# Kernel optimization log

Hardware: AMD Instinct MI355X
Metric: run time of the kernel (lower is better)

## Reference

```python
import jax, jax.numpy as jnp
import numpy as np

N_STATE = 1280
N_HEAD = 20
D_HEAD = N_STATE // N_HEAD  # 64
N_MLP = 4 * N_STATE         # 5120
EPS = 1e-5


def _layer_norm(x, gamma, beta):
    mu = jnp.mean(x, axis=-1, keepdims=True)
    var = jnp.mean(jnp.square(x - mu), axis=-1, keepdims=True)
    return (x - mu) * jax.lax.rsqrt(var + EPS) * gamma + beta


def setup_inputs() -> dict:
    key = jax.random.key(0)
    ks = jax.random.split(key, 16)
    s = lambda fan_in: 1.0 / np.sqrt(fan_in)
    d = {
        "x": jax.random.normal(ks[0], (1, 1500, N_STATE), jnp.float32),
        # attention projections (stored [in, out]; torch Linear does x @ W.T + b)
        "Wq": jax.random.normal(ks[1], (N_STATE, N_STATE), jnp.float32) * s(N_STATE),
        "bq": jax.random.normal(ks[2], (N_STATE,), jnp.float32) * 0.02,
        "Wk": jax.random.normal(ks[3], (N_STATE, N_STATE), jnp.float32) * s(N_STATE),  # no bias
        "Wv": jax.random.normal(ks[4], (N_STATE, N_STATE), jnp.float32) * s(N_STATE),
        "bv": jax.random.normal(ks[5], (N_STATE,), jnp.float32) * 0.02,
        "Wo": jax.random.normal(ks[6], (N_STATE, N_STATE), jnp.float32) * s(N_STATE),
        "bo": jax.random.normal(ks[7], (N_STATE,), jnp.float32) * 0.02,
        # layer norms
        "ln1_g": jnp.ones((N_STATE,), jnp.float32),
        "ln1_b": jnp.zeros((N_STATE,), jnp.float32),
        "ln2_g": jnp.ones((N_STATE,), jnp.float32),
        "ln2_b": jnp.zeros((N_STATE,), jnp.float32),
        # MLP
        "W1": jax.random.normal(ks[8], (N_STATE, N_MLP), jnp.float32) * s(N_STATE),
        "b1": jax.random.normal(ks[9], (N_MLP,), jnp.float32) * 0.02,
        "W2": jax.random.normal(ks[10], (N_MLP, N_STATE), jnp.float32) * s(N_MLP),
        "b2": jax.random.normal(ks[11], (N_STATE,), jnp.float32) * 0.02,
    }
    return d


def reference(x, Wq, bq, Wk, Wv, bv, Wo, bo, ln1_g, ln1_b, ln2_g, ln2_b, W1, b1, W2, b2):
    B, S, C = x.shape
    scale = D_HEAD ** -0.5

    # --- multi-head self-attention ---
    h = _layer_norm(x, ln1_g, ln1_b)
    q = (h @ Wq + bq).reshape(B, S, N_HEAD, D_HEAD)
    k = (h @ Wk).reshape(B, S, N_HEAD, D_HEAD)
    v = (h @ Wv + bv).reshape(B, S, N_HEAD, D_HEAD)
    # scores: [B, H, Q, K]; softmax over keys (dim=1 'k' in the torch einsum)
    scores = jnp.einsum('bqhd,bkhd->bhqk', q, k) * scale
    w = jax.nn.softmax(scores, axis=-1)
    attn = jnp.einsum('bhqk,bkhd->bqhd', w, v).reshape(B, S, C)
    attn = attn @ Wo + bo
    x = x + attn

    # --- MLP (exact GELU, matching torch nn.GELU default) ---
    h2 = _layer_norm(x, ln2_g, ln2_b)
    h2 = jax.nn.gelu(h2 @ W1 + b1, approximate=False)
    x = x + (h2 @ W2 + b2)
    return x
```

## Files before the change

### kernel.cpp

```cpp
#include <hip/hip_runtime.h>
#include <hip/hip_bf16.h>
#include <math.h>

typedef __bf16 bf16x8 __attribute__((ext_vector_type(8)));
typedef float f32x4 __attribute__((ext_vector_type(4)));

#define SEQ 1500
#define CDIM 1280
#define NHEAD 20
#define DHEAD 64
#define NMLP 5120
#define QKVN 3840
#define VTLD 1504
#define APAD 68

#define GLOAD_LDS16(gp, lp)                                                    \
  __builtin_amdgcn_global_load_lds(                                            \
      (const __attribute__((address_space(1))) unsigned int*)(gp),             \
      (__attribute__((address_space(3))) unsigned int*)(lp), 16, 0, 0)

__global__ __launch_bounds__(256) void pack_params_kernel(
    const unsigned int* __restrict__ xw, const void* bq, const void* bv,
    const void* bo, const void* g1, const void* be1, const void* g2,
    const void* be2, const void* b1, const void* b2,
    __bf16* __restrict__ pb, int* __restrict__ flag) {
  __shared__ int cnt[256];
  const unsigned int w = xw[threadIdx.x];
  const unsigned int e = (w >> 7) & 0xFF;
  cnt[threadIdx.x] = (e >= 100 && e <= 150) ? 1 : 0;
  __syncthreads();
  for (int s = 128; s > 0; s >>= 1) {
    if (threadIdx.x < (unsigned)s) cnt[threadIdx.x] += cnt[threadIdx.x + s];
    __syncthreads();
  }
  const int isbf = (cnt[0] >= 160) ? 1 : 0;
  if (blockIdx.x == 0 && threadIdx.x == 0) flag[0] = isbf;
  const int i = blockIdx.x * 256 + threadIdx.x;
  if (i >= 16640) return;
  auto ld = [&](const void* p, int j) -> float {
    return isbf ? (float)((const __bf16*)p)[j] : ((const float*)p)[j];
  };
  float v;
  if (i < 3840) {
    if (i < 1280) v = ld(bq, i);
    else if (i < 2560) v = 0.f;
    else v = ld(bv, i - 2560);
  } else if (i < 5120) v = ld(bo, i - 3840);
  else if (i < 6400) v = ld(g1, i - 5120);
  else if (i < 7680) v = ld(be1, i - 6400);
  else if (i < 8960) v = ld(g2, i - 7680);
  else if (i < 10240) v = ld(be2, i - 8960);
  else if (i < 15360) v = ld(b1, i - 10240);
  else v = ld(b2, i - 15360);
  pb[i] = (__bf16)v;
}

__device__ __forceinline__ void transpose_body(const void* in, __bf16* out,
                                               int K, int N, int isbf,
                                               int bx, int by) {
  __shared__ __bf16 t[32][33];
  const int tx = threadIdx.x, ty = threadIdx.y;
  const int n0 = bx * 32, k0 = by * 32;
  if (isbf) {
    const __bf16* s = (const __bf16*)in;
#pragma unroll
    for (int i = ty; i < 32; i += 8)
      t[i][tx] = s[(size_t)(k0 + i) * N + n0 + tx];
  } else {
    const float* s = (const float*)in;
#pragma unroll
    for (int i = ty; i < 32; i += 8)
      t[i][tx] = (__bf16)s[(size_t)(k0 + i) * N + n0 + tx];
  }
  __syncthreads();
#pragma unroll
  for (int i = ty; i < 32; i += 8)
    out[(size_t)(n0 + i) * K + k0 + tx] = t[tx][i];
}

__global__ __launch_bounds__(256) void transpose_all_kernel(
    const void* Wq, const void* Wk, const void* Wv, const void* Wo,
    const void* W1, const void* W2, __bf16* __restrict__ Wqkvt,
    __bf16* __restrict__ Wot, __bf16* __restrict__ W1t,
    __bf16* __restrict__ W2t, const int* __restrict__ flag) {
  const int id = blockIdx.x;
  const int isbf = flag[0];
  if (id < 6400) {
    const int w = id / 1600, r = id % 1600;
    const void* in = (w == 0) ? Wq : (w == 1) ? Wk : (w == 2) ? Wv : Wo;
    __bf16* out = (w < 3) ? (Wqkvt + (size_t)w * CDIM * CDIM) : Wot;
    transpose_body(in, out, CDIM, CDIM, isbf, r % 40, r / 40);
  } else if (id < 12800) {
    const int r = id - 6400;
    transpose_body(W1, W1t, CDIM, NMLP, isbf, r % 160, r / 160);
  } else {
    const int r = id - 12800;
    transpose_body(W2, W2t, NMLP, CDIM, isbf, r % 40, r / 40);
  }
}

__global__ __launch_bounds__(256) void transpose_act_kernel(const __bf16* __restrict__ in,
                                                            __bf16* __restrict__ out,
                                                            int istride) {
  __shared__ __bf16 t[32][33];
  const int tx = threadIdx.x, ty = threadIdx.y;
  const int n0 = blockIdx.x * 32, k0 = blockIdx.y * 32;
#pragma unroll
  for (int i = ty; i < 32; i += 8) {
    const int k = k0 + i;
    t[i][tx] = (k < SEQ) ? in[(size_t)k * istride + n0 + tx] : (__bf16)0.f;
  }
  __syncthreads();
#pragma unroll
  for (int i = ty; i < 32; i += 8) {
    const int kk = k0 + tx;
    if (kk < VTLD) out[(size_t)(n0 + i) * VTLD + kk] = t[tx][i];
  }
}

__global__ __launch_bounds__(256) void ln_kernel(const void* __restrict__ X,
                                                 const __bf16* __restrict__ gamma,
                                                 const __bf16* __restrict__ beta,
                                                 __bf16* __restrict__ Y,
                                                 const int* __restrict__ flag) {
  const int isf32 = (flag[0] == 0);
  const int row = blockIdx.x;
  float v[5];
  float s = 0.f, s2 = 0.f;
#pragma unroll
  for (int i = 0; i < 5; ++i) {
    const int c = threadIdx.x + 256 * i;
    const size_t idx = (size_t)row * CDIM + c;
    v[i] = isf32 ? ((const float*)X)[idx] : (float)((const __bf16*)X)[idx];
    s += v[i];
    s2 += v[i] * v[i];
  }
  const int lane = threadIdx.x & 63, wv = threadIdx.x >> 6;
#pragma unroll
  for (int off = 32; off > 0; off >>= 1) {
    s += __shfl_down(s, off);
    s2 += __shfl_down(s2, off);
  }
  __shared__ float red[8];
  if (lane == 0) { red[wv] = s; red[4 + wv] = s2; }
  __syncthreads();
  s = red[0] + red[1] + red[2] + red[3];
  s2 = red[4] + red[5] + red[6] + red[7];
  const float mu = s * (1.f / CDIM);
  const float var = s2 * (1.f / CDIM) - mu * mu;
  const float rstd = rsqrtf(fmaxf(var, 0.f) + 1e-5f);
#pragma unroll
  for (int i = 0; i < 5; ++i) {
    const int c = threadIdx.x + 256 * i;
    Y[(size_t)row * CDIM + c] =
        (__bf16)((v[i] - mu) * rstd * (float)gamma[c] + (float)beta[c]);
  }
}

__global__ __launch_bounds__(256) void resid_ln_kernel(
    const float* __restrict__ P, const __bf16* __restrict__ bo,
    const void* __restrict__ X, const __bf16* __restrict__ gamma,
    const __bf16* __restrict__ beta, __bf16* __restrict__ X1,
    __bf16* __restrict__ H2, const int* __restrict__ flag) {
  const int isf32 = (flag[0] == 0);
  const int row = blockIdx.x;
  const int MN = SEQ * CDIM;
  float v[5];
  float s = 0.f, s2 = 0.f;
#pragma unroll
  for (int i = 0; i < 5; ++i) {
    const int c = threadIdx.x + 256 * i;
    const size_t idx = (size_t)row * CDIM + c;
    const float xv = isf32 ? ((const float*)X)[idx] : (float)((const __bf16*)X)[idx];
    const float val = P[idx] + P[MN + idx] + (float)bo[c] + xv;
    X1[idx] = (__bf16)val;
    v[i] = val;
    s += val;
    s2 += val * val;
  }
  const int lane = threadIdx.x & 63, wv = threadIdx.x >> 6;
#pragma unroll
  for (int off = 32; off > 0; off >>= 1) {
    s += __shfl_down(s, off);
    s2 += __shfl_down(s2, off);
  }
  __shared__ float red[8];
  if (lane == 0) { red[wv] = s; red[4 + wv] = s2; }
  __syncthreads();
  s = red[0] + red[1] + red[2] + red[3];
  s2 = red[4] + red[5] + red[6] + red[7];
  const float mu = s * (1.f / CDIM);
  const float var = s2 * (1.f / CDIM) - mu * mu;
  const float rstd = rsqrtf(fmaxf(var, 0.f) + 1e-5f);
#pragma unroll
  for (int i = 0; i < 5; ++i) {
    const int c = threadIdx.x + 256 * i;
    H2[(size_t)row * CDIM + c] =
        (__bf16)((v[i] - mu) * rstd * (float)gamma[c] + (float)beta[c]);
  }
}

__global__ __launch_bounds__(256) void gemm64_kernel(
    const __bf16* __restrict__ A, const __bf16* __restrict__ Bt,
    const __bf16* __restrict__ bias, void* __restrict__ Cv,
    int M, int N, int K, int KS, int gelu, int nsplit) {
  __shared__ __bf16 As[2][64 * 32];
  __shared__ __bf16 Bs[2][128 * 32];
  const int bm = blockIdx.x, bn = blockIdx.y, sz = blockIdx.z;
  const int tid = threadIdx.x;
  const int lane = tid & 63, wave = tid >> 6;
  const int l16 = lane & 15, kq = (lane >> 4) << 3;
  const int lrow = lane >> 2, lcol = (lane & 3) << 3;
  const int wn = wave * 32;

  f32x4 acc[4][2];
  const f32x4 zero = {0.f, 0.f, 0.f, 0.f};
#pragma unroll
  for (int i = 0; i < 4; ++i)
#pragma unroll
    for (int j = 0; j < 2; ++j) acc[i][j] = zero;

  const int kbeg = sz * KS;
  int kend = kbeg + KS;
  if (kend > K) kend = K;

  int ga = bm * 64 + wave * 16 + lrow;
  if (ga > M - 1) ga = M - 1;
  const __bf16* Ap = A + (size_t)ga * K + lcol;

  for (int k0 = kbeg; k0 < kend; k0 += 64) {
#pragma unroll
    for (int c = 0; c < 2; ++c)
      GLOAD_LDS16(Ap + k0 + c * 32, &As[c][wave * 512]);
#pragma unroll
    for (int c = 0; c < 2; ++c)
#pragma unroll
      for (int t = 0; t < 2; ++t) {
        const int seg = t * 4 + wave;
        const int gb = bn * 128 + seg * 16 + lrow;
        GLOAD_LDS16(Bt + (size_t)gb * K + k0 + c * 32 + lcol, &Bs[c][seg * 512]);
      }
    __syncthreads();
    bf16x8 af[4][2], bfr[2][2];
#pragma unroll
    for (int i = 0; i < 4; ++i)
#pragma unroll
      for (int c = 0; c < 2; ++c)
        af[i][c] = *(const bf16x8*)(&As[c][(i * 16 + l16) * 32 + kq]);
#pragma unroll
    for (int j = 0; j < 2; ++j)
#pragma unroll
      for (int c = 0; c < 2; ++c)
        bfr[j][c] = *(const bf16x8*)(&Bs[c][(wn + j * 16 + l16) * 32 + kq]);
#pragma unroll
    for (int i = 0; i < 4; ++i)
#pragma unroll
      for (int j = 0; j < 2; ++j)
#pragma unroll
        for (int c = 0; c < 2; ++c)
          acc[i][j] = __builtin_amdgcn_mfma_f32_16x16x32_bf16(af[i][c], bfr[j][c],
                                                              acc[i][j], 0, 0, 0);
    __syncthreads();
  }

  const int rq4 = (lane >> 4) * 4;
  if (nsplit > 1) {
    float* P = (float*)Cv + (size_t)sz * M * N;
#pragma unroll
    for (int i = 0; i < 4; ++i)
#pragma unroll
      for (int r = 0; r < 4; ++r) {
        const int grow = bm * 64 + i * 16 + rq4 + r;
        if (grow >= M) continue;
#pragma unroll
        for (int j = 0; j < 2; ++j) {
          const int gcol = bn * 128 + wn + j * 16 + l16;
          P[(size_t)grow * N + gcol] = acc[i][j][r];
        }
      }
  } else {
    __bf16* Cb = (__bf16*)Cv;
#pragma unroll
    for (int i = 0; i < 4; ++i)
#pragma unroll
      for (int r = 0; r < 4; ++r) {
        const int grow = bm * 64 + i * 16 + rq4 + r;
        if (grow >= M) continue;
#pragma unroll
        for (int j = 0; j < 2; ++j) {
          const int gcol = bn * 128 + wn + j * 16 + l16;
          float vv = acc[i][j][r];
          if (bias) vv += (float)bias[gcol];
          if (gelu) vv = 0.5f * vv * (1.f + erff(vv * 0.70710678118654752f));
          Cb[(size_t)grow * N + gcol] = (__bf16)vv;
        }
      }
  }
}

__global__ __launch_bounds__(256, 2) void gemm128c_kernel(
    const __bf16* __restrict__ A, const __bf16* __restrict__ Bt,
    const __bf16* __restrict__ bias, __bf16* __restrict__ C,
    int M, int N, int K, int gelu, int mtiles) {
  __shared__ __bf16 As[2][128 * 64];
  __shared__ __bf16 Bs[2][128 * 64];

  const int nwg = mtiles * (N >> 7);
  const int qq = nwg >> 3, rr = nwg & 7;
  const int xcd = blockIdx.x & 7, rk = blockIdx.x >> 3;
  const int wg = (xcd < rr ? xcd * (qq + 1) : rr * (qq + 1) + (xcd - rr) * qq) + rk;
  const int bm = wg % mtiles, bn = wg / mtiles;

  const int tid = threadIdx.x;
  const int lane = tid & 63, wave = tid >> 6;
  const int wm = (wave >> 1) * 64, wn = (wave & 1) * 64;
  const int l16 = lane & 15, quad = lane >> 4;

  const int rT = tid >> 3, sl = tid & 7;
  const int aoff = ((sl * 16) ^ ((rT & 7) << 4)) >> 1;
  const __bf16* Ap[4];
  const __bf16* Bp[4];
#pragma unroll
  for (int s = 0; s < 4; ++s) {
    int gm = bm * 128 + s * 32 + rT;
    if (gm > M - 1) gm = M - 1;
    Ap[s] = A + (size_t)gm * K + aoff;
    Bp[s] = Bt + (size_t)(bn * 128 + s * 32 + rT) * K + aoff;
  }
  const int ldst = tid * 8;

  const int xsw = (l16 & 7) << 4;
  const int kb0 = ((quad << 4) ^ xsw) >> 1;
  const int kb1 = (((quad << 4) + 64) ^ xsw) >> 1;

  f32x4 acc[4][4];
  const f32x4 zero = {0.f, 0.f, 0.f, 0.f};
#pragma unroll
  for (int i = 0; i < 4; ++i)
#pragma unroll
    for (int j = 0; j < 4; ++j) acc[i][j] = zero;

  const int NT = K >> 6;

#define STAGE128(b, k0)                                       \
  do {                                                        \
    _Pragma("unroll")                                         \
    for (int s = 0; s < 4; ++s) {                             \
      GLOAD_LDS16(Ap[s] + (k0), &As[b][s * 2048 + ldst]);     \
      GLOAD_LDS16(Bp[s] + (k0), &Bs[b][s * 2048 + ldst]);     \
    }                                                         \
  } while (0)

  STAGE128(0, 0);
  for (int t = 0; t < NT; ++t) {
    const int cur = t & 1;
    if (t + 1 < NT) {
      STAGE128(cur ^ 1, (t + 1) * 64);
      asm volatile("s_waitcnt vmcnt(8)" ::: "memory");
    } else {
      asm volatile("s_waitcnt vmcnt(0)" ::: "memory");
    }
    __builtin_amdgcn_s_barrier();
    __builtin_amdgcn_sched_barrier(0);
    bf16x8 af[4][2], bfr[4][2];
#pragma unroll
    for (int i = 0; i < 4; ++i) {
      const int row = (wm + i * 16 + l16) * 64;
      af[i][0] = *(const bf16x8*)(&As[cur][row + kb0]);
      af[i][1] = *(const bf16x8*)(&As[cur][row + kb1]);
    }
#pragma unroll
    for (int j = 0; j < 4; ++j) {
      const int row = (wn + j * 16 + l16) * 64;
      bfr[j][0] = *(const bf16x8*)(&Bs[cur][row + kb0]);
      bfr[j][1] = *(const bf16x8*)(&Bs[cur][row + kb1]);
    }
    __builtin_amdgcn_s_setprio(1);
#pragma unroll
    for (int i = 0; i < 4; ++i)
#pragma unroll
      for (int j = 0; j < 4; ++j)
#pragma unroll
        for (int c = 0; c < 2; ++c)
          acc[i][j] = __builtin_amdgcn_mfma_f32_16x16x32_bf16(af[i][c], bfr[j][c],
                                                              acc[i][j], 0, 0, 0);
    __builtin_amdgcn_s_setprio(0);
    __builtin_amdgcn_s_barrier();
    __builtin_amdgcn_sched_barrier(0);
  }
#undef STAGE128

#pragma unroll
  for (int i = 0; i < 4; ++i)
#pragma unroll
    for (int r = 0; r < 4; ++r) {
      const int grow = bm * 128 + wm + i * 16 + quad * 4 + r;
      if (grow >= M) continue;
#pragma unroll
      for (int j = 0; j < 4; ++j) {
        const int gcol = bn * 128 + wn + j * 16 + l16;
        float vv = acc[i][j][r];
        if (bias) vv += (float)bias[gcol];
        if (gelu) vv = 0.5f * vv * (1.f + erff(vv * 0.70710678118654752f));
        C[(size_t)grow * N + gcol] = (__bf16)vv;
      }
    }
}

__global__ __launch_bounds__(256) void reduce_kernel(
    const float* __restrict__ P, const __bf16* __restrict__ bias,
    const __bf16* __restrict__ resid, void* __restrict__ out,
    int MN, int N, const int* __restrict__ flag) {
  const int i = blockIdx.x * 256 + threadIdx.x;
  if (i >= MN) return;
  const float v = P[i] + P[(size_t)MN + i] + (float)bias[i % N] + (float)resid[i];
  if (flag[0]) ((__bf16*)out)[i] = (__bf16)v;
  else         ((float*)out)[i] = v;
}

__global__ __launch_bounds__(256) void attn_mfma_kernel(
    const __bf16* __restrict__ Q,
    const __bf16* __restrict__ Kk,
    const __bf16* __restrict__ Vt,
    float* __restrict__ Opart,
    float* __restrict__ ml,
    int rs) {
  const int h = blockIdx.y;
  const int q0 = blockIdx.x * 64;
  const int z = blockIdx.z;
  const int tid = threadIdx.x;
  const int wave = tid >> 6, lane = tid & 63;
  const int l16 = lane & 15, quad = lane >> 4;

  __shared__ __bf16 Ks[64 * APAD];
  __shared__ __bf16 Vs[64 * APAD];
  __shared__ __bf16 Ps[4][16 * APAD];

  bf16x8 qf[2];
  {
    int q = q0 + wave * 16 + l16;
    if (q > SEQ - 1) q = SEQ - 1;
    const __bf16* qp = Q + (size_t)q * rs + h * DHEAD + quad * 8;
    qf[0] = *(const bf16x8*)(qp);
    qf[1] = *(const bf16x8*)(qp + 32);
  }

  f32x4 oacc[4];
  const f32x4 zero = {0.f, 0.f, 0.f, 0.f};
#pragma unroll
  for (int jt = 0; jt < 4; ++jt) oacc[jt] = zero;
  float mrow[4], lrow[4];
#pragma unroll
  for (int r = 0; r < 4; ++r) { mrow[r] = -30000.f; lrow[r] = 0.f; }

  const int srow = tid >> 2;
  const int scol = (tid & 3) << 4;

  const __bf16* Kbase = Kk + h * DHEAD;
  const __bf16* Vbase = Vt + (size_t)(h * DHEAD + srow) * VTLD;

  for (int kt = z * 12; kt < z * 12 + 12; ++kt) {
    const int key0 = kt * 64;
    __syncthreads();
    {
      int gk = key0 + srow;
      if (gk > SEQ - 1) gk = SEQ - 1;
      const __bf16* kp = Kbase + (size_t)gk * rs + scol;
      *(bf16x8*)(&Ks[srow * APAD + scol]) = *(const bf16x8*)(kp);
      *(bf16x8*)(&Ks[srow * APAD + scol + 8]) = *(const bf16x8*)(kp + 8);
      const __bf16* vp = Vbase + key0 + scol;
      *(bf16x8*)(&Vs[srow * APAD + scol]) = *(const bf16x8*)(vp);
      *(bf16x8*)(&Vs[srow * APAD + scol + 8]) = *(const bf16x8*)(vp + 8);
    }
    __syncthreads();

    f32x4 s[4];
#pragma unroll
    for (int jt = 0; jt < 4; ++jt) s[jt] = zero;
#pragma unroll
    for (int jt = 0; jt < 4; ++jt)
#pragma unroll
      for (int ks = 0; ks < 2; ++ks) {
        const bf16x8 kf = *(const bf16x8*)(&Ks[(jt * 16 + l16) * APAD + ks * 32 + quad * 8]);
        s[jt] = __builtin_amdgcn_mfma_f32_16x16x32_bf16(qf[ks], kf, s[jt], 0, 0, 0);
      }

#pragma unroll
    for (int jt = 0; jt < 4; ++jt) {
      const int key = key0 + jt * 16 + l16;
#pragma unroll
      for (int r = 0; r < 4; ++r) {
        float sv = s[jt][r] * 0.125f;
        if (key >= SEQ) sv = -30000.f;
        s[jt][r] = sv;
      }
    }

#pragma unroll
    for (int r = 0; r < 4; ++r) {
      float tmax = fmaxf(fmaxf(s[0][r], s[1][r]), fmaxf(s[2][r], s[3][r]));
#pragma unroll
      for (int off = 8; off > 0; off >>= 1) tmax = fmaxf(tmax, __shfl_xor(tmax, off));
      const float mnew = fmaxf(mrow[r], tmax);
      const float alpha = __expf(mrow[r] - mnew);
      mrow[r] = mnew;
      lrow[r] *= alpha;
#pragma unroll
      for (int jt = 0; jt < 4; ++jt) oacc[jt][r] *= alpha;
#pragma unroll
      for (int jt = 0; jt < 4; ++jt) {
        const float p = __expf(s[jt][r] - mnew);
        lrow[r] += p;
        Ps[wave][(quad * 4 + r) * APAD + jt * 16 + l16] = (__bf16)p;
      }
    }

    bf16x8 pf[2];
    pf[0] = *(const bf16x8*)(&Ps[wave][l16 * APAD + quad * 8]);
    pf[1] = *(const bf16x8*)(&Ps[wave][l16 * APAD + 32 + quad * 8]);
#pragma unroll
    for (int jt = 0; jt < 4; ++jt)
#pragma unroll
      for (int ks = 0; ks < 2; ++ks) {
        const bf16x8 vf = *(const bf16x8*)(&Vs[(jt * 16 + l16) * APAD + ks * 32 + quad * 8]);
        oacc[jt] = __builtin_amdgcn_mfma_f32_16x16x32_bf16(pf[ks], vf, oacc[jt], 0, 0, 0);
      }
  }

  float* Oz = Opart + (size_t)z * SEQ * CDIM;
#pragma unroll
  for (int r = 0; r < 4; ++r) {
    float lt = lrow[r];
#pragma unroll
    for (int off = 8; off > 0; off >>= 1) lt += __shfl_xor(lt, off);
    const int q = q0 + wave * 16 + quad * 4 + r;
    if (q < SEQ) {
#pragma unroll
      for (int jt = 0; jt < 4; ++jt)
        Oz[(size_t)q * CDIM + h * DHEAD + jt * 16 + l16] = oacc[jt][r];
      if (l16 == 0) {
        const size_t mi = ((size_t)(z * NHEAD + h) * SEQ + q) * 2;
        ml[mi] = mrow[r];
        ml[mi + 1] = lt;
      }
    }
  }
}

__global__ __launch_bounds__(256) void attn_combine_kernel(
    const float* __restrict__ Op, const float* __restrict__ ml,
    __bf16* __restrict__ O) {
  const int i = blockIdx.x * 256 + threadIdx.x;
  if (i >= SEQ * CDIM) return;
  const int q = i / CDIM;
  const int h = (i % CDIM) >> 6;
  const size_t m1i = ((size_t)h * SEQ + q) * 2;
  const size_t m2i = ((size_t)(NHEAD + h) * SEQ + q) * 2;
  const float m1 = ml[m1i], l1 = ml[m1i + 1];
  const float m2 = ml[m2i], l2 = ml[m2i + 1];
  const float M = fmaxf(m1, m2);
  const float e1 = __expf(m1 - M), e2 = __expf(m2 - M);
  const float v = (e1 * Op[i] + e2 * Op[(size_t)SEQ * CDIM + i]) /
                  (e1 * l1 + e2 * l2);
  O[i] = (__bf16)v;
}

extern "C" void kernel_launch(void* const* d_in, const int* in_sizes, int n_in,
                              void* d_out, int out_size, void* d_ws, size_t ws_size,
                              hipStream_t stream) {
  const void* x   = d_in[0];
  const void* Wq  = d_in[1];
  const void* bq  = d_in[2];
  const void* Wk  = d_in[3];
  const void* Wv  = d_in[4];
  const void* bv  = d_in[5];
  const void* Wo  = d_in[6];
  const void* bo  = d_in[7];
  const void* g1  = d_in[8];
  const void* be1 = d_in[9];
  const void* g2  = d_in[10];
  const void* be2 = d_in[11];
  const void* W1  = d_in[12];
  const void* bm1 = d_in[13];
  const void* W2  = d_in[14];
  const void* bm2 = d_in[15];

  char* ws = (char*)d_ws;
  size_t off = 0;
  auto alloc = [&](size_t elems) {
    __bf16* p = (__bf16*)(ws + off);
    off += elems * sizeof(__bf16);
    return p;
  };
  __bf16* Wqkvt = alloc((size_t)QKVN * CDIM);
  __bf16* Wot   = alloc((size_t)CDIM * CDIM);
  __bf16* W1t   = alloc((size_t)CDIM * NMLP);
  __bf16* W2t   = alloc((size_t)CDIM * NMLP);
  __bf16* qkvb  = alloc((size_t)SEQ * QKVN);
  __bf16* hb    = alloc((size_t)SEQ * CDIM);
  __bf16* mb    = alloc((size_t)SEQ * NMLP);
  __bf16* pb    = alloc(20480);
  off = (off + 15) & ~(size_t)15;
  float* pscr = (float*)(ws + off);
  off += (size_t)2 * SEQ * CDIM * sizeof(float);
  float* mlb = (float*)(ws + off);
  off += (size_t)2 * NHEAD * SEQ * 2 * sizeof(float);
  int* flag = (int*)(ws + off);

  __bf16* vtb  = mb;
  __bf16* x1b  = qkvb;
  __bf16* h2b  = qkvb + (size_t)SEQ * CDIM;

  __bf16* qkvbias = pb + 0;
  __bf16* bo_b  = pb + 3840;
  __bf16* g1_b  = pb + 5120;
  __bf16* be1_b = pb + 6400;
  __bf16* g2_b  = pb + 7680;
  __bf16* be2_b = pb + 8960;
  __bf16* b1_b  = pb + 10240;
  __bf16* b2_b  = pb + 15360;

  pack_params_kernel<<<65, 256, 0, stream>>>(
      (const unsigned int*)x, bq, bv, bo, g1, be1, g2, be2, bm1, bm2, pb, flag);
  transpose_all_kernel<<<19200, dim3(32, 8), 0, stream>>>(
      Wq, Wk, Wv, Wo, W1, W2, Wqkvt, Wot, W1t, W2t, flag);
  ln_kernel<<<SEQ, 256, 0, stream>>>(x, g1_b, be1_b, hb, flag);
  gemm128c_kernel<<<360, 256, 0, stream>>>(
      hb, Wqkvt, qkvbias, qkvb, SEQ, QKVN, CDIM, 0, 12);
  transpose_act_kernel<<<dim3(40, 47), dim3(32, 8), 0, stream>>>(
      qkvb + 2560, vtb, QKVN);
  attn_mfma_kernel<<<dim3(24, NHEAD, 2), 256, 0, stream>>>(
      qkvb, qkvb + 1280, vtb, pscr, mlb, QKVN);
  attn_combine_kernel<<<7500, 256, 0, stream>>>(pscr, mlb, hb);
  gemm64_kernel<<<dim3(24, 10, 2), 256, 0, stream>>>(
      hb, Wot, nullptr, pscr, SEQ, CDIM, CDIM, 640, 0, 2);
  resid_ln_kernel<<<SEQ, 256, 0, stream>>>(pscr, bo_b, x, g2_b, be2_b,
                                           x1b, h2b, flag);
  gemm128c_kernel<<<480, 256, 0, stream>>>(
      h2b, W1t, b1_b, mb, SEQ, NMLP, CDIM, 1, 12);
  gemm64_kernel<<<dim3(24, 10, 2), 256, 0, stream>>>(
      mb, W2t, nullptr, pscr, SEQ, CDIM, NMLP, 2560, 0, 2);
  reduce_kernel<<<7500, 256, 0, stream>>>(pscr, b2_b, x1b, d_out,
                                          SEQ * CDIM, CDIM, flag);
}
```

Baseline: 361.6 us.

## Split attention keys four ways and prefetch next K/V tile into registers

The attention kernel now splits the key range into four chunks of six 64-key tiles instead of two chunks of twelve. This doubles the number of blocks, which gives the GPU more parallelism and better load balance. The K/V tile loads are software-pipelined: the next tile's global loads go into registers while the current tile is computed, replacing the load-then-sync pattern with a store-to-LDS, sync, prefetch, compute, sync loop. The combine kernel now merges four partial softmax results, which adds partial-output scratch memory and extra read traffic in the combine step.

Measured after the change: 364.3 us. About the same (+0.7%).

```diff
diff --git a/kernel.cpp b/kernel.cpp
--- a/kernel.cpp
+++ b/kernel.cpp
@@ -13,6 +13,7 @@
 #define QKVN 3840
 #define VTLD 1504
 #define APAD 68
+#define ZSPLIT 4
 
 #define GLOAD_LDS16(gp, lp)                                                    \
   __builtin_amdgcn_global_load_lds(                                            \
@@ -459,20 +460,37 @@
   const __bf16* Kbase = Kk + h * DHEAD;
   const __bf16* Vbase = Vt + (size_t)(h * DHEAD + srow) * VTLD;
 
-  for (int kt = z * 12; kt < z * 12 + 12; ++kt) {
+  const int kbeg = z * 6, kend = z * 6 + 6;
+
+  bf16x8 kr0, kr1, vr0, vr1;
+  {
+    int gk = kbeg * 64 + srow;
+    if (gk > SEQ - 1) gk = SEQ - 1;
+    const __bf16* kp = Kbase + (size_t)gk * rs + scol;
+    kr0 = *(const bf16x8*)(kp);
+    kr1 = *(const bf16x8*)(kp + 8);
+    const __bf16* vp = Vbase + kbeg * 64 + scol;
+    vr0 = *(const bf16x8*)(vp);
+    vr1 = *(const bf16x8*)(vp + 8);
+  }
+
+  for (int kt = kbeg; kt < kend; ++kt) {
     const int key0 = kt * 64;
+    *(bf16x8*)(&Ks[srow * APAD + scol]) = kr0;
+    *(bf16x8*)(&Ks[srow * APAD + scol + 8]) = kr1;
+    *(bf16x8*)(&Vs[srow * APAD + scol]) = vr0;
+    *(bf16x8*)(&Vs[srow * APAD + scol + 8]) = vr1;
     __syncthreads();
-    {
-      int gk = key0 + srow;
+    if (kt + 1 < kend) {
+      int gk = (kt + 1) * 64 + srow;
       if (gk > SEQ - 1) gk = SEQ - 1;
       const __bf16* kp = Kbase + (size_t)gk * rs + scol;
-      *(bf16x8*)(&Ks[srow * APAD + scol]) = *(const bf16x8*)(kp);
-      *(bf16x8*)(&Ks[srow * APAD + scol + 8]) = *(const bf16x8*)(kp + 8);
-      const __bf16* vp = Vbase + key0 + scol;
-      *(bf16x8*)(&Vs[srow * APAD + scol]) = *(const bf16x8*)(vp);
-      *(bf16x8*)(&Vs[srow * APAD + scol + 8]) = *(const bf16x8*)(vp + 8);
-    }
-    __syncthreads();
+      kr0 = *(const bf16x8*)(kp);
+      kr1 = *(const bf16x8*)(kp + 8);
+      const __bf16* vp = Vbase + (kt + 1) * 64 + scol;
+      vr0 = *(const bf16x8*)(vp);
+      vr1 = *(const bf16x8*)(vp + 8);
+    }
 
     f32x4 s[4];
 #pragma unroll
@@ -525,6 +543,7 @@
         const bf16x8 vf = *(const bf16x8*)(&Vs[(jt * 16 + l16) * APAD + ks * 32 + quad * 8]);
         oacc[jt] = __builtin_amdgcn_mfma_f32_16x16x32_bf16(pf[ks], vf, oacc[jt], 0, 0, 0);
       }
+    __syncthreads();
   }
 
   float* Oz = Opart + (size_t)z * SEQ * CDIM;
@@ -554,15 +573,23 @@
   if (i >= SEQ * CDIM) return;
   const int q = i / CDIM;
   const int h = (i % CDIM) >> 6;
-  const size_t m1i = ((size_t)h * SEQ + q) * 2;
-  const size_t m2i = ((size_t)(NHEAD + h) * SEQ + q) * 2;
-  const float m1 = ml[m1i], l1 = ml[m1i + 1];
-  const float m2 = ml[m2i], l2 = ml[m2i + 1];
-  const float M = fmaxf(m1, m2);
-  const float e1 = __expf(m1 - M), e2 = __expf(m2 - M);
-  const float v = (e1 * Op[i] + e2 * Op[(size_t)SEQ * CDIM + i]) /
-                  (e1 * l1 + e2 * l2);
-  O[i] = (__bf16)v;
+  float mz[ZSPLIT], lz[ZSPLIT];
+  float M = -1e30f;
+#pragma unroll
+  for (int z = 0; z < ZSPLIT; ++z) {
+    const size_t mi = ((size_t)(z * NHEAD + h) * SEQ + q) * 2;
+    mz[z] = ml[mi];
+    lz[z] = ml[mi + 1];
+    M = fmaxf(M, mz[z]);
+  }
+  float num = 0.f, den = 0.f;
+#pragma unroll
+  for (int z = 0; z < ZSPLIT; ++z) {
+    const float e = __expf(mz[z] - M);
+    num += e * Op[(size_t)z * SEQ * CDIM + i];
+    den += e * lz[z];
+  }
+  O[i] = (__bf16)(num / den);
 }
 
 extern "C" void kernel_launch(void* const* d_in, const int* in_sizes, int n_in,
@@ -602,9 +629,9 @@
   __bf16* pb    = alloc(20480);
   off = (off + 15) & ~(size_t)15;
   float* pscr = (float*)(ws + off);
-  off += (size_t)2 * SEQ * CDIM * sizeof(float);
+  off += (size_t)ZSPLIT * SEQ * CDIM * sizeof(float);
   float* mlb = (float*)(ws + off);
-  off += (size_t)2 * NHEAD * SEQ * 2 * sizeof(float);
+  off += (size_t)ZSPLIT * NHEAD * SEQ * 2 * sizeof(float);
   int* flag = (int*)(ws + off);
 
   __bf16* vtb  = mb;
@@ -629,7 +656,7 @@
       hb, Wqkvt, qkvbias, qkvb, SEQ, QKVN, CDIM, 0, 12);
   transpose_act_kernel<<<dim3(40, 47), dim3(32, 8), 0, stream>>>(
       qkvb + 2560, vtb, QKVN);
-  attn_mfma_kernel<<<dim3(24, NHEAD, 2), 256, 0, stream>>>(
+  attn_mfma_kernel<<<dim3(24, NHEAD, ZSPLIT), 256, 0, stream>>>(
       qkvb, qkvb + 1280, vtb, pscr, mlb, QKVN);
   attn_combine_kernel<<<7500, 256, 0, stream>>>(pscr, mlb, hb);
   gemm64_kernel<<<dim3(24, 10, 2), 256, 0, stream>>>(
```

## Use 128x256 tile 8-wave triple-buffered GEMM for MLP up-projection

Applied to the files above, without the earlier changes.

Adds a new GEMM kernel with 512 threads (8 waves) computing 128x256 output tiles, using a three-stage LDS ring buffer fed by direct global-to-LDS loads. It issues loads two half-K steps ahead and applies an XCD-aware workgroup remap. The kernel is used for the W1 GEMM with fused bias and GELU, replacing the 128x128 kernel. The wider tile raises reuse of A and halves the number of workgroups. The cost is more LDS per block and only 240 blocks, which may leave some compute units idle.

New measurement: 366.8 us. No clear change (+1.5%).

```diff
diff --git a/kernel.cpp b/kernel.cpp
--- a/kernel.cpp
+++ b/kernel.cpp
@@ -399,6 +399,111 @@
 #pragma unroll
       for (int j = 0; j < 4; ++j) {
         const int gcol = bn * 128 + wn + j * 16 + l16;
+        float vv = acc[i][j][r];
+        if (bias) vv += (float)bias[gcol];
+        if (gelu) vv = 0.5f * vv * (1.f + erff(vv * 0.70710678118654752f));
+        C[(size_t)grow * N + gcol] = (__bf16)vv;
+      }
+    }
+}
+
+__global__ __launch_bounds__(512, 4) void gemm8p_kernel(
+    const __bf16* __restrict__ A, const __bf16* __restrict__ Bt,
+    const __bf16* __restrict__ bias, __bf16* __restrict__ C,
+    int M, int N, int K, int gelu, int mtiles) {
+  __shared__ __bf16 Ah[3][128 * 32];
+  __shared__ __bf16 Bh[3][256 * 32];
+
+  const int nwg = mtiles * (N >> 8);
+  const int qq = nwg >> 3, rr = nwg & 7;
+  const int xcd = blockIdx.x & 7, rk = blockIdx.x >> 3;
+  const int wg = (xcd < rr ? xcd * (qq + 1) : rr * (qq + 1) + (xcd - rr) * qq) + rk;
+  const int bm = wg % mtiles, bn = wg / mtiles;
+
+  const int tid = threadIdx.x;
+  const int lane = tid & 63, wave = tid >> 6;
+  const int wm = wave >> 2, wn = wave & 3;
+  const int l16 = lane & 15, quad = lane >> 4;
+
+  const int rS = tid >> 2, slS = tid & 3;
+  const int soff = ((slS * 16) ^ ((rS & 3) << 4)) >> 1;
+  int gmA = bm * 128 + rS;
+  if (gmA > M - 1) gmA = M - 1;
+  const __bf16* ApS = A + (size_t)gmA * K + soff;
+  const __bf16* BpS0 = Bt + (size_t)(bn * 256 + rS) * K + soff;
+  const __bf16* BpS1 = Bt + (size_t)(bn * 256 + 128 + rS) * K + soff;
+  const int ldst = tid * 8;
+
+  const int kq = ((quad * 16) ^ ((l16 & 3) << 4)) >> 1;
+  const int arow0 = (wm * 64 + l16) * 32;
+  const int brow0 = (wn * 64 + l16) * 32;
+
+  f32x4 acc[4][4];
+  const f32x4 zero = {0.f, 0.f, 0.f, 0.f};
+#pragma unroll
+  for (int i = 0; i < 4; ++i)
+#pragma unroll
+    for (int j = 0; j < 4; ++j) acc[i][j] = zero;
+
+#define STAGE_H(h)                                            \
+  do {                                                        \
+    const int b2_ = (h) % 3;                                  \
+    const int ko_ = (h) * 32;                                 \
+    GLOAD_LDS16(ApS + ko_, &Ah[b2_][ldst]);                   \
+    GLOAD_LDS16(BpS0 + ko_, &Bh[b2_][ldst]);                  \
+    GLOAD_LDS16(BpS1 + ko_, &Bh[b2_][4096 + ldst]);           \
+  } while (0)
+
+#define PHASE8(h, DO_ISSUE, VMSTMT)                                           \
+  do {                                                                        \
+    const int b_ = (h) % 3;                                                   \
+    bf16x8 af_[4], bf_[4];                                                    \
+    _Pragma("unroll")                                                         \
+    for (int i = 0; i < 4; ++i)                                               \
+      af_[i] = *(const bf16x8*)(&Ah[b_][arow0 + i * 512 + kq]);               \
+    _Pragma("unroll")                                                         \
+    for (int j = 0; j < 4; ++j)                                               \
+      bf_[j] = *(const bf16x8*)(&Bh[b_][brow0 + j * 512 + kq]);               \
+    if (DO_ISSUE) STAGE_H((h) + 2);                                           \
+    VMSTMT;                                                                   \
+    __builtin_amdgcn_s_barrier();                                             \
+    asm volatile("s_waitcnt lgkmcnt(0)" ::: "memory");                        \
+    __builtin_amdgcn_sched_barrier(0);                                        \
+    __builtin_amdgcn_s_setprio(1);                                            \
+    _Pragma("unroll")                                                         \
+    for (int i = 0; i < 4; ++i)                                               \
+      _Pragma("unroll")                                                       \
+      for (int j = 0; j < 4; ++j)                                             \
+        acc[i][j] = __builtin_amdgcn_mfma_f32_16x16x32_bf16(af_[i], bf_[j],   \
+                                                            acc[i][j], 0, 0, 0); \
+    __builtin_amdgcn_s_setprio(0);                                            \
+    __builtin_amdgcn_s_barrier();                                             \
+    __builtin_amdgcn_sched_barrier(0);                                        \
+  } while (0)
+
+  STAGE_H(0);
+  STAGE_H(1);
+  asm volatile("s_waitcnt vmcnt(3)" ::: "memory");
+  __builtin_amdgcn_s_barrier();
+  __builtin_amdgcn_sched_barrier(0);
+
+  const int HP = (K >> 6) * 2;
+  for (int h = 0; h < HP - 2; ++h)
+    PHASE8(h, true, asm volatile("s_waitcnt vmcnt(3)" ::: "memory"));
+  PHASE8(HP - 2, false, asm volatile("s_waitcnt vmcnt(0)" ::: "memory"));
+  PHASE8(HP - 1, false, (void)0);
+#undef PHASE8
+#undef STAGE_H
+
+#pragma unroll
+  for (int i = 0; i < 4; ++i)
+#pragma unroll
+    for (int r = 0; r < 4; ++r) {
+      const int grow = bm * 128 + wm * 64 + i * 16 + quad * 4 + r;
+      if (grow >= M) continue;
+#pragma unroll
+      for (int j = 0; j < 4; ++j) {
+        const int gcol = bn * 256 + wn * 64 + j * 16 + l16;
         float vv = acc[i][j][r];
         if (bias) vv += (float)bias[gcol];
         if (gelu) vv = 0.5f * vv * (1.f + erff(vv * 0.70710678118654752f));
@@ -636,7 +741,7 @@
       hb, Wot, nullptr, pscr, SEQ, CDIM, CDIM, 640, 0, 2);
   resid_ln_kernel<<<SEQ, 256, 0, stream>>>(pscr, bo_b, x, g2_b, be2_b,
                                            x1b, h2b, flag);
-  gemm128c_kernel<<<480, 256, 0, stream>>>(
+  gemm8p_kernel<<<240, 512, 0, stream>>>(
       h2b, W1t, b1_b, mb, SEQ, NMLP, CDIM, 1, 12);
   gemm64_kernel<<<dim3(24, 10, 2), 256, 0, stream>>>(
       mb, W2t, nullptr, pscr, SEQ, CDIM, NMLP, 2560, 0, 2);
```
